# Kernel optimization log

Measured on AMD Instinct MI355X. Metric: run time of the kernel, lower is better.

Reference implementation:

```python
import jax, jax.numpy as jnp
import numpy as np

B, S, H, L = 4096, 64, 768, 5
TEMP = 0.07
BN_EPS = 1e-5


def setup_inputs() -> dict:
    key = jax.random.key(0)
    ks = jax.random.split(key, 8)
    seq = jax.random.normal(ks[0], (B, S, H), dtype=jnp.float32)
    labels = jax.random.randint(ks[1], (B,), 0, L)
    s = 1.0 / np.sqrt(H)
    return {
        'sequence_output': seq,
        'cls_gamma': jnp.ones((H,), jnp.float32),
        'cls_beta': jnp.zeros((H,), jnp.float32),
        'cls_W': jax.random.normal(ks[2], (H, H), jnp.float32) * s,
        'cls_b': jax.random.normal(ks[3], (H,), jnp.float32) * 0.01,
        'label_gamma': jnp.ones((H,), jnp.float32),
        'label_beta': jnp.zeros((H,), jnp.float32),
        'label_W': jax.random.normal(ks[4], (H, H), jnp.float32) * s,
        'label_b': jax.random.normal(ks[5], (H,), jnp.float32) * 0.01,
        'labels': labels,
    }


def _batchnorm(x, gamma, beta):
    # training-mode BatchNorm1d: biased batch stats
    m = x.mean(0)
    v = jnp.mean((x - m) ** 2, axis=0)
    return (x - m) * jax.lax.rsqrt(v + BN_EPS) * gamma + beta


def _l2norm(x):
    return x / jnp.sqrt(jnp.sum(x * x, axis=-1, keepdims=True)).clip(1e-12)


def reference(sequence_output, cls_gamma, cls_beta, cls_W, cls_b,
              label_gamma, label_beta, label_W, label_b, labels):
    z = sequence_output[:, 0, :]  # [B,H]; dropout is identity in eval
    # label token spans: 'No relation' -> positions 1:3 (mean), rest single tokens 3..6
    theta = jnp.stack([
        sequence_output[:, 1:3, :].mean(axis=1),
        sequence_output[:, 3, :],
        sequence_output[:, 4, :],
        sequence_output[:, 5, :],
        sequence_output[:, 6, :],
    ], axis=1)  # [B,L,H]
    z_cl, theta_cl = z, theta

    zp = _batchnorm(z, cls_gamma, cls_beta) @ cls_W.T + cls_b  # [B,H]
    tp = _batchnorm(theta.reshape(-1, H), label_gamma, label_beta) @ label_W.T + label_b
    tp = tp.reshape(-1, L, H)  # [B,L,H]
    logits = jnp.einsum('blh,bh->bl', tp, zp)  # [B,L]

    # ---- dual supervised contrastive loss (vectorized over the python loops) ----
    z_norm = _l2norm(z_cl)        # [B,H]
    theta_norm = _l2norm(theta_cl)  # [B,L,H]
    same = labels[:, None] == labels[None, :]          # [B,B]
    eye = jnp.eye(labels.shape[0], dtype=bool)
    pos_mask = (same & ~eye).astype(jnp.float32)       # positives (same label, j != i)
    neg_mask = (~same).astype(jnp.float32)             # negatives (different label)
    has_pos = (same & ~eye).any(axis=1)

    # l_z: anchor z_i vs theta_j[labels_i] (pos) and all theta_j[:] for diff-label j (neg)
    expS = jnp.exp(jnp.einsum('ih,jlh->ijl', z_norm, theta_norm) / TEMP)  # [B,B,L]
    expS_at_lab = jnp.take_along_axis(
        expS, jnp.broadcast_to(labels[:, None, None], expS.shape[:2] + (1,)), axis=2
    )[..., 0]  # expS[i,j,labels[i]] -> [B,B]
    pos_z = jnp.sum(expS_at_lab * pos_mask, axis=1)
    neg_z = jnp.sum(expS.sum(axis=-1) * neg_mask, axis=1)
    l_z = jnp.where(has_pos, -jnp.log(pos_z / (pos_z + neg_z + 1e-8)), 0.0).sum()

    # l_theta: anchor theta_i[labels_i] vs z_j
    anchor_theta = jnp.take_along_axis(theta_norm, labels[:, None, None], axis=1)[:, 0, :]  # [B,H]
    expT = jnp.exp(anchor_theta @ z_norm.T / TEMP)  # [B,B]
    pos_t = jnp.sum(expT * pos_mask, axis=1)
    neg_t = jnp.sum(expT * neg_mask, axis=1)
    l_t = jnp.where(has_pos, -jnp.log(pos_t / (pos_t + neg_t + 1e-8)), 0.0).sum()

    dual_loss = (l_z + l_t) / labels.shape[0]
    return logits, dual_loss
```

## Files before the change

### kernel.cpp

```cpp
#include <hip/hip_runtime.h>
#include <hip/hip_bf16.h>
#include <cstdint>
#include <cstddef>

#define B_N 4096
#define S_N 64
#define H_N 768
#define L_N 5
#define TEMP_INV (1.0f / 0.07f)
#define BN_EPS 1e-5f

typedef __attribute__((ext_vector_type(8))) short short8;
typedef __attribute__((ext_vector_type(4))) float f32x4;

__device__ __forceinline__ void async_copy16(void* lds, const void* g) {
  __builtin_amdgcn_global_load_lds(
      (const __attribute__((address_space(1))) unsigned int*)g,
      (__attribute__((address_space(3))) unsigned int*)lds, 16, 0, 0);
}

__device__ __forceinline__ unsigned short bf16b(float x) {
  __hip_bfloat16 h = __float2bfloat16(x);
  return *reinterpret_cast<unsigned short*>(&h);
}
__device__ __forceinline__ void store_bf16x4(void* p, float4 v) {
  ushort4 o = make_ushort4(bf16b(v.x), bf16b(v.y), bf16b(v.z), bf16b(v.w));
  *reinterpret_cast<ushort4*>(p) = o;
}

__device__ inline float block_reduce_sum256(float v, float* sbuf) {
#pragma unroll
  for (int off = 32; off > 0; off >>= 1) v += __shfl_down(v, off, 64);
  int lane = threadIdx.x & 63;
  int wid = threadIdx.x >> 6;
  __syncthreads();
  if (lane == 0) sbuf[wid] = v;
  __syncthreads();
  float r = 0.f;
  if (threadIdx.x == 0) r = sbuf[0] + sbuf[1] + sbuf[2] + sbuf[3];
  return r;
}

__global__ __launch_bounds__(256) void extract_kernel(
    const float* __restrict__ seq, __hip_bfloat16* __restrict__ zb,
    __hip_bfloat16* __restrict__ tb, float* __restrict__ zn_inv,
    float* __restrict__ thn_inv, float* __restrict__ sum_z,
    float* __restrict__ ssq_z, float* __restrict__ sum_t,
    float* __restrict__ ssq_t) {
  __shared__ float pr[16][6][3];
  int t = threadIdx.x;
  int wv = t >> 6, ln = t & 63;
  bool act = t < 192;
  int c4 = t * 4;
  int b0 = blockIdx.x * 16;
  float zs[4] = {}, zq[4] = {}, ts4[4] = {}, tq4[4] = {};
  for (int r = 0; r < 16; ++r) {
    int b = b0 + r;
    const float* base = seq + (size_t)b * (S_N * H_N);
    float pv[6] = {0.f, 0.f, 0.f, 0.f, 0.f, 0.f};
    if (act) {
      float4 z4 = *(const float4*)(base + c4);
      store_bf16x4(zb + (size_t)b * H_N + c4, z4);
      pv[0] = z4.x * z4.x + z4.y * z4.y + z4.z * z4.z + z4.w * z4.w;
      zs[0] += z4.x; zs[1] += z4.y; zs[2] += z4.z; zs[3] += z4.w;
      zq[0] += z4.x * z4.x; zq[1] += z4.y * z4.y;
      zq[2] += z4.z * z4.z; zq[3] += z4.w * z4.w;
#pragma unroll
      for (int l = 0; l < L_N; ++l) {
        float4 v4;
        if (l == 0) {
          float4 a4 = *(const float4*)(base + H_N + c4);
          float4 b4 = *(const float4*)(base + 2 * H_N + c4);
          v4 = make_float4(0.5f * (a4.x + b4.x), 0.5f * (a4.y + b4.y),
                           0.5f * (a4.z + b4.z), 0.5f * (a4.w + b4.w));
        } else {
          v4 = *(const float4*)(base + (size_t)(l + 2) * H_N + c4);
        }
        store_bf16x4(tb + ((size_t)b * L_N + l) * H_N + c4, v4);
        pv[1 + l] = v4.x * v4.x + v4.y * v4.y + v4.z * v4.z + v4.w * v4.w;
        ts4[0] += v4.x; ts4[1] += v4.y; ts4[2] += v4.z; ts4[3] += v4.w;
        tq4[0] += v4.x * v4.x; tq4[1] += v4.y * v4.y;
        tq4[2] += v4.z * v4.z; tq4[3] += v4.w * v4.w;
      }
    }
#pragma unroll
    for (int v = 0; v < 6; ++v) {
      float x = pv[v];
#pragma unroll
      for (int off = 32; off > 0; off >>= 1) x += __shfl_down(x, off, 64);
      if (ln == 0 && wv < 3) pr[r][v][wv] = x;
    }
  }
  __syncthreads();
  if (t < 96) {
    int r = t / 6, v = t - r * 6;
    float s = pr[r][v][0] + pr[r][v][1] + pr[r][v][2];
    float inv = 1.f / fmaxf(sqrtf(s), 1e-12f);
    int b = b0 + r;
    if (v == 0) zn_inv[b] = inv;
    else thn_inv[b * L_N + (v - 1)] = inv;
  }
  if (act) {
#pragma unroll
    for (int j = 0; j < 4; ++j) {
      atomicAdd(&sum_z[c4 + j], zs[j]);
      atomicAdd(&ssq_z[c4 + j], zq[j]);
      atomicAdd(&sum_t[c4 + j], ts4[j]);
      atomicAdd(&ssq_t[c4 + j], tq4[j]);
    }
  }
}

__global__ void count_kernel(const int* __restrict__ labels, int* __restrict__ cnt) {
  int i = blockIdx.x * 256 + threadIdx.x;
  if (i < B_N) atomicAdd(&cnt[labels[i]], 1);
}

__global__ void finalize_kernel(
    const float* __restrict__ sum_z, const float* __restrict__ ssq_z,
    const float* __restrict__ sum_t, const float* __restrict__ ssq_t,
    const float* __restrict__ g_z, const float* __restrict__ b_z,
    const float* __restrict__ g_t, const float* __restrict__ b_t,
    float* __restrict__ sz_s, float* __restrict__ sz_t,
    float* __restrict__ st_s, float* __restrict__ st_t) {
  int h = blockIdx.x * 256 + threadIdx.x;
  if (h >= H_N) return;
  {
    float m = sum_z[h] * (1.f / B_N);
    float v = ssq_z[h] * (1.f / B_N) - m * m;
    float s = g_z[h] * rsqrtf(v + BN_EPS);
    sz_s[h] = s;
    sz_t[h] = b_z[h] - m * s;
  }
  {
    float m = sum_t[h] * (1.f / (B_N * L_N));
    float v = ssq_t[h] * (1.f / (B_N * L_N)) - m * m;
    float s = g_t[h] * rsqrtf(v + BN_EPS);
    st_s[h] = s;
    st_t[h] = b_t[h] - m * s;
  }
}

__global__ __launch_bounds__(256) void prep_cls_kernel(
    const float* __restrict__ W, const float* __restrict__ szs,
    const float* __restrict__ szt, const float* __restrict__ bias,
    __hip_bfloat16* __restrict__ Wb, float* __restrict__ cprime) {
  __shared__ float sbuf[4];
  int n = blockIdx.x;
  int t = threadIdx.x;
  float dot = 0.f;
  if (t < 192) {
    int c4 = t * 4;
    const float* row = W + (size_t)n * H_N;
    float4 w4 = *(const float4*)(row + c4);
    float4 s4 = *(const float4*)(szs + c4);
    float4 t4 = *(const float4*)(szt + c4);
    store_bf16x4(Wb + (size_t)n * H_N + c4,
                 make_float4(w4.x * s4.x, w4.y * s4.y, w4.z * s4.z, w4.w * s4.w));
    dot = w4.x * t4.x + w4.y * t4.y + w4.z * t4.z + w4.w * t4.w;
  }
  float s = block_reduce_sum256(dot, sbuf);
  if (t == 0) cprime[n] = s + bias[n];
}

__global__ __launch_bounds__(256) void transpose_wl_kernel(
    const float* __restrict__ Wl, __hip_bfloat16* __restrict__ WlT) {
  __shared__ float tile[32][33];
  int t = threadIdx.x;
  int tx = t & 31, ty0 = t >> 5;
  int n0 = blockIdx.x * 32, k0 = blockIdx.y * 32;
#pragma unroll
  for (int p = 0; p < 4; ++p)
    tile[ty0 + p * 8][tx] = Wl[(size_t)(n0 + ty0 + p * 8) * H_N + k0 + tx];
  __syncthreads();
#pragma unroll
  for (int p = 0; p < 4; ++p) {
    unsigned short us = bf16b(tile[tx][ty0 + p * 8]);
    *((unsigned short*)WlT + (size_t)(k0 + ty0 + p * 8) * H_N + n0 + tx) = us;
  }
}

template <bool WRITE_BF16, bool HAS_BIAS>
__global__ __launch_bounds__(256) void gemm128_kernel(
    const __hip_bfloat16* __restrict__ A, const __hip_bfloat16* __restrict__ Bm,
    const float* __restrict__ bias, float* __restrict__ outF,
    __hip_bfloat16* __restrict__ outB) {
  __shared__ __align__(16) __hip_bfloat16 Asm[128 * 32];
  __shared__ __align__(16) __hip_bfloat16 Bsm[128 * 32];
  int tid = threadIdx.x, lane = tid & 63, wid = tid >> 6;
  int wr = wid >> 1, wc = wid & 1;
  int i0 = blockIdx.x * 128, n0 = blockIdx.y * 128;
  int llo = lane & 15, lhi = lane >> 4;
  f32x4 acc[4][4] = {};
  for (int k0 = 0; k0 < H_N; k0 += 32) {
#pragma unroll
    for (int r = 0; r < 2; ++r) {
      int s = r * 256 + wid * 64 + lane;
      int row = s >> 2, kc = (s & 3) * 8;
      size_t go = (size_t)row * H_N + k0 + kc;
      async_copy16((char*)Asm + (size_t)(r * 256 + wid * 64) * 16,
                   A + (size_t)i0 * H_N + go);
      async_copy16((char*)Bsm + (size_t)(r * 256 + wid * 64) * 16,
                   Bm + (size_t)n0 * H_N + go);
    }
    __syncthreads();
    short8 a[4], b[4];
#pragma unroll
    for (int m = 0; m < 4; ++m)
      a[m] = *(const short8*)((const char*)Asm +
                              ((wr * 64 + m * 16 + llo) * 32 + lhi * 8) * 2);
#pragma unroll
    for (int n = 0; n < 4; ++n)
      b[n] = *(const short8*)((const char*)Bsm +
                              ((wc * 64 + n * 16 + llo) * 32 + lhi * 8) * 2);
#pragma unroll
    for (int m = 0; m < 4; ++m)
#pragma unroll
      for (int n = 0; n < 4; ++n)
        acc[m][n] =
            __builtin_amdgcn_mfma_f32_16x16x32_bf16(a[m], b[n], acc[m][n], 0, 0, 0);
    __syncthreads();
  }
#pragma unroll
  for (int n = 0; n < 4; ++n) {
    int col = n0 + wc * 64 + n * 16 + llo;
    float bv = HAS_BIAS ? bias[col] : 0.f;
#pragma unroll
    for (int m = 0; m < 4; ++m) {
#pragma unroll
      for (int r = 0; r < 4; ++r) {
        int row = i0 + wr * 64 + m * 16 + lhi * 4 + r;
        float val = acc[m][n][r] + bv;
        outF[(size_t)row * H_N + col] = val;
        if (WRITE_BF16)
          outB[(size_t)row * H_N + col] = __float2bfloat16(val);
      }
    }
  }
}

__global__ __launch_bounds__(256) void logits_kernel(
    const float* __restrict__ seq, const float* __restrict__ u,
    const float* __restrict__ zp, const float* __restrict__ st_s,
    const float* __restrict__ st_t, const float* __restrict__ label_b,
    float* __restrict__ out) {
  __shared__ float sbuf[4];
  int b = blockIdx.x;
  int t = threadIdx.x;
  bool act = t < 192;
  int c4 = t * 4;
  float4 w4 = make_float4(0.f, 0.f, 0.f, 0.f);
  float apart = 0.f;
  if (act) {
    float4 u4 = *(const float4*)(u + (size_t)b * H_N + c4);
    float4 zp4 = *(const float4*)(zp + (size_t)b * H_N + c4);
    float4 ss4 = *(const float4*)(st_s + c4);
    float4 tt4 = *(const float4*)(st_t + c4);
    float4 lb4 = *(const float4*)(label_b + c4);
    w4 = make_float4(u4.x * ss4.x, u4.y * ss4.y, u4.z * ss4.z, u4.w * ss4.w);
    apart = u4.x * tt4.x + u4.y * tt4.y + u4.z * tt4.z + u4.w * tt4.w +
            zp4.x * lb4.x + zp4.y * lb4.y + zp4.z * lb4.z + zp4.w * lb4.w;
  }
  float alpha = block_reduce_sum256(apart, sbuf);
  const float* base = seq + (size_t)b * (S_N * H_N);
#pragma unroll
  for (int l = 0; l < L_N; ++l) {
    float part = 0.f;
    if (act) {
      float4 v4;
      if (l == 0) {
        float4 a4 = *(const float4*)(base + H_N + c4);
        float4 b4 = *(const float4*)(base + 2 * H_N + c4);
        v4 = make_float4(0.5f * (a4.x + b4.x), 0.5f * (a4.y + b4.y),
                         0.5f * (a4.z + b4.z), 0.5f * (a4.w + b4.w));
      } else {
        v4 = *(const float4*)(base + (size_t)(l + 2) * H_N + c4);
      }
      part = v4.x * w4.x + v4.y * w4.y + v4.z * w4.z + v4.w * w4.w;
    }
    float s = block_reduce_sum256(part, sbuf);
    if (t == 0) out[b * L_N + l] = s + alpha;
  }
}

__global__ __launch_bounds__(256) void sgemm_fused_kernel(
    const __hip_bfloat16* __restrict__ zb, const __hip_bfloat16* __restrict__ tb,
    const float* __restrict__ zn_inv, const float* __restrict__ thn_inv,
    const int* __restrict__ labels, float* __restrict__ pos_z,
    float* __restrict__ neg_z, float* __restrict__ pos_t,
    float* __restrict__ neg_t) {
  __shared__ __align__(16) __hip_bfloat16 Asm[128 * 32];
  __shared__ __align__(16) __hip_bfloat16 Bsm[128 * 32];
  __shared__ float rpos[128], rneg[128], cpos[128], cneg[128];
  __shared__ float rnorm[128], cnorm[128];
  __shared__ int rowlab[128], colj[128], coll[128], collab[128];

  int tid = threadIdx.x;
  int lane = tid & 63, wid = tid >> 6;
  int wr = wid >> 1, wc = wid & 1;
  int i0 = blockIdx.x * 128, n0 = blockIdx.y * 128;
  int llo = lane & 15, lhi = lane >> 4;

  f32x4 acc[4][4] = {};

  for (int k0 = 0; k0 < H_N; k0 += 32) {
#pragma unroll
    for (int r = 0; r < 2; ++r) {
      int s = r * 256 + wid * 64 + lane;
      int row = s >> 2, kc = (s & 3) * 8;
      size_t go = (size_t)row * H_N + k0 + kc;
      async_copy16((char*)Asm + (size_t)(r * 256 + wid * 64) * 16,
                   zb + (size_t)i0 * H_N + go);
      async_copy16((char*)Bsm + (size_t)(r * 256 + wid * 64) * 16,
                   tb + (size_t)n0 * H_N + go);
    }
    __syncthreads();
    short8 a[4], b[4];
#pragma unroll
    for (int m = 0; m < 4; ++m)
      a[m] = *(const short8*)((const char*)Asm +
                              ((wr * 64 + m * 16 + llo) * 32 + lhi * 8) * 2);
#pragma unroll
    for (int n = 0; n < 4; ++n)
      b[n] = *(const short8*)((const char*)Bsm +
                              ((wc * 64 + n * 16 + llo) * 32 + lhi * 8) * 2);
#pragma unroll
    for (int m = 0; m < 4; ++m)
#pragma unroll
      for (int n = 0; n < 4; ++n)
        acc[m][n] =
            __builtin_amdgcn_mfma_f32_16x16x32_bf16(a[m], b[n], acc[m][n], 0, 0, 0);
    __syncthreads();
  }

  if (tid < 128) {
    rowlab[tid] = labels[i0 + tid];
    rnorm[tid] = zn_inv[i0 + tid] * TEMP_INV;
    int c = n0 + tid;
    int j = c / 5;
    colj[tid] = j;
    coll[tid] = c - j * 5;
    collab[tid] = labels[j];
    cnorm[tid] = thn_inv[c];
    rpos[tid] = 0.f; rneg[tid] = 0.f; cpos[tid] = 0.f; cneg[tid] = 0.f;
  }
  __syncthreads();

  int cl[4], jg[4], lv[4], lj[4];
  float cs[4];
#pragma unroll
  for (int n = 0; n < 4; ++n) {
    cl[n] = wc * 64 + n * 16 + llo;
    jg[n] = colj[cl[n]];
    lv[n] = coll[cl[n]];
    lj[n] = collab[cl[n]];
    cs[n] = cnorm[cl[n]];
  }
  float cpAcc[4] = {}, cnAcc[4] = {};
#pragma unroll
  for (int m = 0; m < 4; ++m) {
#pragma unroll
    for (int r = 0; r < 4; ++r) {
      int rl = wr * 64 + m * 16 + lhi * 4 + r;
      int ig = i0 + rl;
      int li = rowlab[rl];
      float rscale = rnorm[rl];
      float rp = 0.f, rn = 0.f;
#pragma unroll
      for (int n = 0; n < 4; ++n) {
        float e = __expf(acc[m][n][r] * rscale * cs[n]);
        bool same = (li == lj[n]);
        bool diag = (ig == jg[n]);
        if (same) {
          if (!diag && lv[n] == li) { rp += e; cpAcc[n] += e; }
        } else {
          rn += e;
          if (lv[n] == lj[n]) cnAcc[n] += e;
        }
      }
      if (rp != 0.f) atomicAdd(&rpos[rl], rp);
      if (rn != 0.f) atomicAdd(&rneg[rl], rn);
    }
  }
#pragma unroll
  for (int n = 0; n < 4; ++n) {
    if (cpAcc[n] != 0.f) atomicAdd(&cpos[cl[n]], cpAcc[n]);
    if (cnAcc[n] != 0.f) atomicAdd(&cneg[cl[n]], cnAcc[n]);
  }
  __syncthreads();
  if (tid < 128) {
    float v;
    v = rpos[tid]; if (v != 0.f) atomicAdd(&pos_z[i0 + tid], v);
    v = rneg[tid]; if (v != 0.f) atomicAdd(&neg_z[i0 + tid], v);
    int j = colj[tid];
    v = cpos[tid]; if (v != 0.f) atomicAdd(&pos_t[j], v);
    v = cneg[tid]; if (v != 0.f) atomicAdd(&neg_t[j], v);
  }
}

__global__ __launch_bounds__(256) void loss_kernel(
    const float* __restrict__ pos_z, const float* __restrict__ neg_z,
    const float* __restrict__ pos_t, const float* __restrict__ neg_t,
    const int* __restrict__ labels, const int* __restrict__ cnt,
    float* __restrict__ out_loss) {
  __shared__ float sbuf[4];
  int i = blockIdx.x * 256 + threadIdx.x;
  float term = 0.f;
  int li = labels[i];
  if (cnt[li] > 1) {
    float pz = pos_z[i], nz = neg_z[i];
    float pt = pos_t[i], nt = neg_t[i];
    term = -logf(pz / (pz + nz + 1e-8f)) - logf(pt / (pt + nt + 1e-8f));
  }
  float s = block_reduce_sum256(term, sbuf);
  if (threadIdx.x == 0) atomicAdd(out_loss, s * (1.0f / B_N));
}

extern "C" void kernel_launch(void* const* d_in, const int* in_sizes, int n_in,
                              void* d_out, int out_size, void* d_ws, size_t ws_size,
                              hipStream_t stream) {
  const float* seq = (const float*)d_in[0];
  const float* cls_gamma = (const float*)d_in[1];
  const float* cls_beta = (const float*)d_in[2];
  const float* cls_W = (const float*)d_in[3];
  const float* cls_b = (const float*)d_in[4];
  const float* label_gamma = (const float*)d_in[5];
  const float* label_beta = (const float*)d_in[6];
  const float* label_W = (const float*)d_in[7];
  const float* label_b = (const float*)d_in[8];
  const int* labels = (const int*)d_in[9];
  float* out = (float*)d_out;
  float* ws = (float*)d_ws;

  constexpr size_t OFF_SUMZ = 0;
  constexpr size_t OFF_SSQZ = 768;
  constexpr size_t OFF_SUMT = 1536;
  constexpr size_t OFF_SSQT = 2304;
  constexpr size_t OFF_POSZ = 3072;
  constexpr size_t OFF_NEGZ = 7168;
  constexpr size_t OFF_POST = 11264;
  constexpr size_t OFF_NEGT = 15360;
  constexpr size_t OFF_CNT = 19456;
  constexpr size_t ZERO_FLOATS = 19464;
  constexpr size_t OFF_SZS = 19464;
  constexpr size_t OFF_SZT = 20232;
  constexpr size_t OFF_STS = 21000;
  constexpr size_t OFF_STT = 21768;
  constexpr size_t OFF_ZNI = 22536;
  constexpr size_t OFF_TNI = 26632;
  constexpr size_t OFF_CPRIME = 47112;
  constexpr size_t OFF_ZP = 47880;
  constexpr size_t OFF_U = OFF_ZP + (size_t)B_N * H_N;
  constexpr size_t F32_END = OFF_U + (size_t)B_N * H_N;
  constexpr size_t BYTE_ZB = F32_END * sizeof(float);
  constexpr size_t BYTE_TB = BYTE_ZB + (size_t)B_N * H_N * 2;
  constexpr size_t BYTE_ZPB = BYTE_TB + (size_t)B_N * L_N * H_N * 2;
  constexpr size_t BYTE_WCB = BYTE_ZPB + (size_t)B_N * H_N * 2;
  constexpr size_t BYTE_WLT = BYTE_WCB + (size_t)H_N * H_N * 2;
  constexpr size_t TOTAL_BYTES = BYTE_WLT + (size_t)H_N * H_N * 2;
  if (ws_size < TOTAL_BYTES) return;

  __hip_bfloat16* zb = (__hip_bfloat16*)((char*)d_ws + BYTE_ZB);
  __hip_bfloat16* tb = (__hip_bfloat16*)((char*)d_ws + BYTE_TB);
  __hip_bfloat16* zpb = (__hip_bfloat16*)((char*)d_ws + BYTE_ZPB);
  __hip_bfloat16* wcb = (__hip_bfloat16*)((char*)d_ws + BYTE_WCB);
  __hip_bfloat16* wlt = (__hip_bfloat16*)((char*)d_ws + BYTE_WLT);

  hipMemsetAsync(d_ws, 0, ZERO_FLOATS * sizeof(float), stream);
  hipMemsetAsync((char*)d_out + (size_t)B_N * L_N * sizeof(float), 0, sizeof(float),
                 stream);

  extract_kernel<<<256, 256, 0, stream>>>(seq, zb, tb, ws + OFF_ZNI, ws + OFF_TNI,
                                          ws + OFF_SUMZ, ws + OFF_SSQZ,
                                          ws + OFF_SUMT, ws + OFF_SSQT);
  count_kernel<<<16, 256, 0, stream>>>(labels, (int*)(ws + OFF_CNT));
  finalize_kernel<<<3, 256, 0, stream>>>(
      ws + OFF_SUMZ, ws + OFF_SSQZ, ws + OFF_SUMT, ws + OFF_SSQT, cls_gamma,
      cls_beta, label_gamma, label_beta, ws + OFF_SZS, ws + OFF_SZT, ws + OFF_STS,
      ws + OFF_STT);
  prep_cls_kernel<<<H_N, 256, 0, stream>>>(cls_W, ws + OFF_SZS, ws + OFF_SZT, cls_b,
                                           wcb, ws + OFF_CPRIME);
  transpose_wl_kernel<<<dim3(24, 24), 256, 0, stream>>>(label_W, wlt);
  gemm128_kernel<true, true><<<dim3(32, 6), 256, 0, stream>>>(
      zb, wcb, ws + OFF_CPRIME, ws + OFF_ZP, zpb);
  gemm128_kernel<false, false><<<dim3(32, 6), 256, 0, stream>>>(
      zpb, wlt, nullptr, ws + OFF_U, nullptr);
  logits_kernel<<<B_N, 256, 0, stream>>>(seq, ws + OFF_U, ws + OFF_ZP, ws + OFF_STS,
                                         ws + OFF_STT, label_b, out);
  sgemm_fused_kernel<<<dim3(32, 160), 256, 0, stream>>>(
      zb, tb, ws + OFF_ZNI, ws + OFF_TNI, labels, ws + OFF_POSZ, ws + OFF_NEGZ,
      ws + OFF_POST, ws + OFF_NEGT);
  loss_kernel<<<16, 256, 0, stream>>>(ws + OFF_POSZ, ws + OFF_NEGZ, ws + OFF_POST,
                                      ws + OFF_NEGT, labels,
                                      (const int*)(ws + OFF_CNT),
                                      out + (size_t)B_N * L_N);
}
```

Measured before the change: 502.6 us.

## Retile similarity GEMM to 256x256 blocks with double-buffered swizzled LDS pipeline

The fused contrastive similarity GEMM moves from 128x128 tiles with 256 threads and a single-buffered K=32 loop to 256x256 tiles with 512 threads. It now uses a K=64 double-buffered async global-to-LDS pipeline with XOR-swizzled LDS layout and raised MFMA priority. The goal is better data reuse per load, fewer LDS bank conflicts, and overlap of loads with MFMA work. In exchange it needs 128KB LDS and many accumulator registers, so only one block fits per CU, and the epilogue buffers reuse the LDS tile memory.

```diff
diff --git a/kernel.cpp b/kernel.cpp
--- a/kernel.cpp
+++ b/kernel.cpp
@@ -283,57 +283,94 @@
   }
 }
 
-__global__ __launch_bounds__(256) void sgemm_fused_kernel(
+#define NT_K 12
+__global__ __launch_bounds__(512, 1) void sgemm_fused_kernel(
     const __hip_bfloat16* __restrict__ zb, const __hip_bfloat16* __restrict__ tb,
     const float* __restrict__ zn_inv, const float* __restrict__ thn_inv,
     const int* __restrict__ labels, float* __restrict__ pos_z,
     float* __restrict__ neg_z, float* __restrict__ pos_t,
     float* __restrict__ neg_t) {
-  __shared__ __align__(16) __hip_bfloat16 Asm[128 * 32];
-  __shared__ __align__(16) __hip_bfloat16 Bsm[128 * 32];
-  __shared__ float rpos[128], rneg[128], cpos[128], cneg[128];
-  __shared__ float rnorm[128], cnorm[128];
-  __shared__ int rowlab[128], colj[128], coll[128], collab[128];
-
-  int tid = threadIdx.x;
-  int lane = tid & 63, wid = tid >> 6;
-  int wr = wid >> 1, wc = wid & 1;
-  int i0 = blockIdx.x * 128, n0 = blockIdx.y * 128;
-  int llo = lane & 15, lhi = lane >> 4;
-
-  f32x4 acc[4][4] = {};
-
-  for (int k0 = 0; k0 < H_N; k0 += 32) {
-#pragma unroll
-    for (int r = 0; r < 2; ++r) {
-      int s = r * 256 + wid * 64 + lane;
-      int row = s >> 2, kc = (s & 3) * 8;
-      size_t go = (size_t)row * H_N + k0 + kc;
-      async_copy16((char*)Asm + (size_t)(r * 256 + wid * 64) * 16,
-                   zb + (size_t)i0 * H_N + go);
-      async_copy16((char*)Bsm + (size_t)(r * 256 + wid * 64) * 16,
-                   tb + (size_t)n0 * H_N + go);
-    }
-    __syncthreads();
-    short8 a[4], b[4];
-#pragma unroll
-    for (int m = 0; m < 4; ++m)
-      a[m] = *(const short8*)((const char*)Asm +
-                              ((wr * 64 + m * 16 + llo) * 32 + lhi * 8) * 2);
-#pragma unroll
-    for (int n = 0; n < 4; ++n)
-      b[n] = *(const short8*)((const char*)Bsm +
-                              ((wc * 64 + n * 16 + llo) * 32 + lhi * 8) * 2);
-#pragma unroll
-    for (int m = 0; m < 4; ++m)
-#pragma unroll
-      for (int n = 0; n < 4; ++n)
-        acc[m][n] =
-            __builtin_amdgcn_mfma_f32_16x16x32_bf16(a[m], b[n], acc[m][n], 0, 0, 0);
-    __syncthreads();
-  }
-
-  if (tid < 128) {
+  __shared__ __align__(128) char ldsbuf[2][65536];
+
+  const int tid = threadIdx.x;
+  const int lane = tid & 63, wid = tid >> 6;
+  const int llo = lane & 15, lhi = lane >> 4;
+  const int wrbase = (wid >> 2) * 128;
+  const int wcbase = (wid & 3) * 64;
+  const int i0 = blockIdx.x * 256, n0 = blockIdx.y * 256;
+  const int wvb = wid << 10;
+
+  f32x4 acc[8][4] = {};
+
+  auto stage = [&](int c, int kt) {
+    char* dA = &ldsbuf[c][0];
+    char* dB = &ldsbuf[c][32768];
+#pragma unroll
+    for (int w = 0; w < 4; ++w) {
+      int s = w * 512 + tid;
+      int row = s >> 3;
+      int lq = (s & 7) ^ (row & 7);
+      int kofs = kt * 64 + lq * 8;
+      async_copy16(dA + w * 8192 + wvb, zb + (size_t)(i0 + row) * H_N + kofs);
+      async_copy16(dB + w * 8192 + wvb, tb + (size_t)(n0 + row) * H_N + kofs);
+    }
+  };
+
+  stage(0, 0);
+  stage(1, 1);
+  asm volatile("s_waitcnt vmcnt(8)" ::: "memory");
+  __builtin_amdgcn_s_barrier();
+
+  for (int t = 0; t < NT_K; ++t) {
+    const char* ldsA = &ldsbuf[t & 1][0];
+    const char* ldsB = &ldsbuf[t & 1][32768];
+#pragma unroll
+    for (int ks = 0; ks < 2; ++ks) {
+      short8 a[8], b[4];
+      int slot = ((ks * 4 + lhi) ^ (llo & 7)) * 16;
+#pragma unroll
+      for (int mi = 0; mi < 8; ++mi) {
+        int row = wrbase + mi * 16 + llo;
+        a[mi] = *(const short8*)(ldsA + row * 128 + slot);
+      }
+#pragma unroll
+      for (int ni = 0; ni < 4; ++ni) {
+        int col = wcbase + ni * 16 + llo;
+        b[ni] = *(const short8*)(ldsB + col * 128 + slot);
+      }
+      __builtin_amdgcn_s_setprio(1);
+#pragma unroll
+      for (int mi = 0; mi < 8; ++mi)
+#pragma unroll
+        for (int ni = 0; ni < 4; ++ni)
+          acc[mi][ni] = __builtin_amdgcn_mfma_f32_16x16x32_bf16(a[mi], b[ni],
+                                                                acc[mi][ni], 0, 0, 0);
+      __builtin_amdgcn_s_setprio(0);
+    }
+    asm volatile("s_waitcnt lgkmcnt(0)" ::: "memory");
+    __builtin_amdgcn_s_barrier();
+    if (t < NT_K - 2) {
+      stage(t & 1, t + 2);
+      asm volatile("s_waitcnt vmcnt(8)" ::: "memory");
+    } else {
+      asm volatile("s_waitcnt vmcnt(0)" ::: "memory");
+    }
+    __builtin_amdgcn_s_barrier();
+  }
+  __syncthreads();
+
+  float* rpos = (float*)&ldsbuf[0][0];
+  float* rneg = rpos + 256;
+  float* cpos = rneg + 256;
+  float* cneg = cpos + 256;
+  float* rnorm = cneg + 256;
+  float* cnorm = rnorm + 256;
+  int* rowlab = (int*)(cnorm + 256);
+  int* colj = rowlab + 256;
+  int* coll = colj + 256;
+  int* collab = coll + 256;
+
+  if (tid < 256) {
     rowlab[tid] = labels[i0 + tid];
     rnorm[tid] = zn_inv[i0 + tid] * TEMP_INV;
     int c = n0 + tid;
@@ -349,33 +386,33 @@
   int cl[4], jg[4], lv[4], lj[4];
   float cs[4];
 #pragma unroll
-  for (int n = 0; n < 4; ++n) {
-    cl[n] = wc * 64 + n * 16 + llo;
-    jg[n] = colj[cl[n]];
-    lv[n] = coll[cl[n]];
-    lj[n] = collab[cl[n]];
-    cs[n] = cnorm[cl[n]];
+  for (int ni = 0; ni < 4; ++ni) {
+    cl[ni] = wcbase + ni * 16 + llo;
+    jg[ni] = colj[cl[ni]];
+    lv[ni] = coll[cl[ni]];
+    lj[ni] = collab[cl[ni]];
+    cs[ni] = cnorm[cl[ni]];
   }
   float cpAcc[4] = {}, cnAcc[4] = {};
 #pragma unroll
-  for (int m = 0; m < 4; ++m) {
+  for (int mi = 0; mi < 8; ++mi) {
 #pragma unroll
     for (int r = 0; r < 4; ++r) {
-      int rl = wr * 64 + m * 16 + lhi * 4 + r;
+      int rl = wrbase + mi * 16 + lhi * 4 + r;
       int ig = i0 + rl;
       int li = rowlab[rl];
       float rscale = rnorm[rl];
       float rp = 0.f, rn = 0.f;
 #pragma unroll
-      for (int n = 0; n < 4; ++n) {
-        float e = __expf(acc[m][n][r] * rscale * cs[n]);
-        bool same = (li == lj[n]);
-        bool diag = (ig == jg[n]);
+      for (int ni = 0; ni < 4; ++ni) {
+        float e = __expf(acc[mi][ni][r] * rscale * cs[ni]);
+        bool same = (li == lj[ni]);
+        bool diag = (ig == jg[ni]);
         if (same) {
-          if (!diag && lv[n] == li) { rp += e; cpAcc[n] += e; }
+          if (!diag && lv[ni] == li) { rp += e; cpAcc[ni] += e; }
         } else {
           rn += e;
-          if (lv[n] == lj[n]) cnAcc[n] += e;
+          if (lv[ni] == lj[ni]) cnAcc[ni] += e;
         }
       }
       if (rp != 0.f) atomicAdd(&rpos[rl], rp);
@@ -383,12 +420,12 @@
     }
   }
 #pragma unroll
-  for (int n = 0; n < 4; ++n) {
-    if (cpAcc[n] != 0.f) atomicAdd(&cpos[cl[n]], cpAcc[n]);
-    if (cnAcc[n] != 0.f) atomicAdd(&cneg[cl[n]], cnAcc[n]);
-  }
-  __syncthreads();
-  if (tid < 128) {
+  for (int ni = 0; ni < 4; ++ni) {
+    if (cpAcc[ni] != 0.f) atomicAdd(&cpos[cl[ni]], cpAcc[ni]);
+    if (cnAcc[ni] != 0.f) atomicAdd(&cneg[cl[ni]], cnAcc[ni]);
+  }
+  __syncthreads();
+  if (tid < 256) {
     float v;
     v = rpos[tid]; if (v != 0.f) atomicAdd(&pos_z[i0 + tid], v);
     v = rneg[tid]; if (v != 0.f) atomicAdd(&neg_z[i0 + tid], v);
@@ -487,7 +524,7 @@
       zpb, wlt, nullptr, ws + OFF_U, nullptr);
   logits_kernel<<<B_N, 256, 0, stream>>>(seq, ws + OFF_U, ws + OFF_ZP, ws + OFF_STS,
                                          ws + OFF_STT, label_b, out);
-  sgemm_fused_kernel<<<dim3(32, 160), 256, 0, stream>>>(
+  sgemm_fused_kernel<<<dim3(16, 80), 512, 0, stream>>>(
       zb, tb, ws + OFF_ZNI, ws + OFF_TNI, labels, ws + OFF_POSZ, ws + OFF_NEGZ,
       ws + OFF_POST, ws + OFF_NEGT);
   loss_kernel<<<16, 256, 0, stream>>>(ws + OFF_POSZ, ws + OFF_NEGZ, ws + OFF_POST,
```

Result: faster. 469.1 us (-6.7%).
